# Kernel optimization log

Hardware: AMD Instinct MI355X
Metric: run time of the kernel (lower is better)

The kernel has to match this reference:

```python
import jax, jax.numpy as jnp
import numpy as np

GAMMA = 1.0
T = 2.0
EPS = 1e-8

def setup_inputs() -> dict:
    key = jax.random.key(0)
    k1, k2 = jax.random.split(key)
    N, D = 8192, 64
    user_vecs = jax.random.normal(k1, (N, D), dtype=jnp.float32)
    item_vecs = jax.random.normal(k2, (N, D), dtype=jnp.float32)
    return {"user_vecs": user_vecs, "item_vecs": item_vecs}

def _normalize(x):
    return x / jnp.linalg.norm(x, axis=-1, keepdims=True)

def _alignment(u, i):
    u = _normalize(u)
    i = _normalize(i)
    return jnp.mean(jnp.sum((u - i) ** 2, axis=1))

def _uniformity(x):
    # log( mean_{i<j} exp(-t * ||x_i - x_j||^2) + eps ) with normalized x.
    # For unit vectors ||x_i - x_j||^2 = 2 - 2 <x_i, x_j>. Use full symmetric
    # Gram matrix: sum over off-diagonal = 2 * sum over i<j; diag contributes
    # exp(0) = 1 per row, so subtract N, divide by N*(N-1).
    x = _normalize(x)
    n = x.shape[0]
    gram = x @ x.T                       # [N, N]
    sq_pdist = jnp.maximum(2.0 - 2.0 * gram, 0.0)
    total = jnp.sum(jnp.exp(-T * sq_pdist))
    mean_pair = (total - n) / (n * (n - 1))
    return jnp.log(mean_pair + EPS)

def reference(user_vecs, item_vecs):
    align = _alignment(user_vecs, item_vecs)
    uniform = GAMMA * (_uniformity(user_vecs) + _uniformity(item_vecs)) / 2.0
    return align + uniform
```

## Files before the change

### kernel.cpp

```cpp
#include <hip/hip_runtime.h>
#include <cstdint>


#define NROWS 8192
#define DIM 64
#define NT2 32
#define GRAM_SLOTS (NT2 * (NT2 + 1))
#define K1_BLOCKS 512

static constexpr float EXP_SCALE = 5.770780163555852f;
static constexpr float EPS_F = 1e-8f;

typedef __bf16 bf16x8 __attribute__((ext_vector_type(8)));
typedef float f32x4 __attribute__((ext_vector_type(4)));

__device__ __forceinline__ unsigned short f32_to_bf16_rn(float f) {
    union { float f; uint32_t u; } c; c.f = f;
    uint32_t u = c.u;
    uint32_t r = u + 0x7FFFu + ((u >> 16) & 1u);
    return (unsigned short)(r >> 16);
}

__global__ void __launch_bounds__(256) normalize_align_kernel(
    const float* __restrict__ user, const float* __restrict__ item,
    unsigned short* __restrict__ xu, unsigned short* __restrict__ xi,
    float* __restrict__ pa)
{
    const int wave = threadIdx.x >> 6;
    const int lane = threadIdx.x & 63;
    const int wid  = blockIdx.x * 4 + wave;

    float asum = 0.0f;
    #pragma unroll
    for (int r = 0; r < 4; ++r) {
        const int idx = (wid * 4 + r) * DIM + lane;
        float u = user[idx];
        float v = item[idx];
        float su = u * u, sv = v * v;
        #pragma unroll
        for (int m = 1; m < 64; m <<= 1) {
            su += __shfl_xor(su, m, 64);
            sv += __shfl_xor(sv, m, 64);
        }
        float iu = rsqrtf(su); iu = iu * (1.5f - 0.5f * su * iu * iu);
        float iv = rsqrtf(sv); iv = iv * (1.5f - 0.5f * sv * iv * iv);
        float un = u * iu, vn = v * iv;
        xu[idx] = f32_to_bf16_rn(un);
        xi[idx] = f32_to_bf16_rn(vn);
        float d = un - vn;
        asum += d * d;
    }
    #pragma unroll
    for (int m = 1; m < 64; m <<= 1) asum += __shfl_xor(asum, m, 64);
    __shared__ float ws4[4];
    if (lane == 0) ws4[wave] = asum;
    __syncthreads();
    if (threadIdx.x == 0) pa[blockIdx.x] = ws4[0] + ws4[1] + ws4[2] + ws4[3];
}

__global__ void __launch_bounds__(512, 8) gram_exp_kernel(
    const unsigned short* __restrict__ xu,
    const unsigned short* __restrict__ xi,
    float* __restrict__ pg)
{
    const int bx = blockIdx.x, by = blockIdx.y;
    const unsigned short* __restrict__ X;
    int bi, bj;
    if (by < NT2) {
        if (by >= bx) { X = xu; bi = bx; bj = by; }
        else          { X = xi; bi = by; bj = bx; }
    } else            { X = xi; bi = bx; bj = bx; }
    const bool diag = (bi == bj);

    __shared__ unsigned short lds[16384];
    __shared__ float wsum[8];

    const int wave = threadIdx.x >> 6;
    const int lane = threadIdx.x & 63;

    bf16x8 a[2][2];
    {
        const int arow = bi * 256 + wave * 32 + (lane & 15);
        const int acol = (lane >> 4) * 8;
        #pragma unroll
        for (int rb = 0; rb < 2; ++rb)
            #pragma unroll
            for (int ks = 0; ks < 2; ++ks)
                a[rb][ks] = *reinterpret_cast<const bf16x8*>(
                    X + (arow + rb * 16) * DIM + acol + ks * 32);
    }

    {
        const int base = bj * 256;
        #pragma unroll
        for (int i = 0; i < 4; ++i) {
            int n = i * 512 + threadIdx.x;
            int r = n >> 3, c = n & 7;
            bf16x8 v = *reinterpret_cast<const bf16x8*>(X + (base + r) * DIM + c * 8);
            int di = (r >> 4) * 1024 + c * 128 + (r & 15) * 8;
            *reinterpret_cast<bf16x8*>(&lds[di]) = v;
        }
    }
    __syncthreads();

    float l0 = 0.0f, l1 = 0.0f;
    #pragma unroll
    for (int cb = 0; cb < 16; ++cb) {
        bf16x8 b0 = *reinterpret_cast<const bf16x8*>(&lds[cb * 1024 + lane * 8]);
        bf16x8 b1 = *reinterpret_cast<const bf16x8*>(&lds[cb * 1024 + 512 + lane * 8]);
        #pragma unroll
        for (int rb = 0; rb < 2; ++rb) {
            f32x4 c = {0.f, 0.f, 0.f, 0.f};
            c = __builtin_amdgcn_mfma_f32_16x16x32_bf16(a[rb][0], b0, c, 0, 0, 0);
            c = __builtin_amdgcn_mfma_f32_16x16x32_bf16(a[rb][1], b1, c, 0, 0, 0);
            #pragma unroll
            for (int e = 0; e < 4; ++e) {
                float ex = __builtin_amdgcn_exp2f(fmaf(c[e], EXP_SCALE, -EXP_SCALE));
                if (diag) ex = fminf(ex, 1.0f);
                if (e & 1) l1 += ex; else l0 += ex;
            }
        }
    }

    float local = l0 + l1;
    #pragma unroll
    for (int m = 1; m < 64; m <<= 1) local += __shfl_xor(local, m, 64);
    if (lane == 0) wsum[wave] = local;
    __syncthreads();
    if (threadIdx.x == 0) {
        float t = 0.f;
        #pragma unroll
        for (int w = 0; w < 8; ++w) t += wsum[w];
        pg[by * NT2 + bx] = diag ? t : 2.0f * t;
    }
}

__global__ void __launch_bounds__(256) final_kernel(
    const float* __restrict__ pa, const float* __restrict__ pg,
    float* __restrict__ out)
{
    float a = 0.f, su = 0.f, si = 0.f;
    for (int s = threadIdx.x; s < K1_BLOCKS; s += 256) a += pa[s];
    for (int s = threadIdx.x; s < GRAM_SLOTS; s += 256) {
        int bx = s & (NT2 - 1), by = s >> 5;
        bool is_item = (by == NT2) || (by < bx);
        float v = pg[s];
        if (is_item) si += v; else su += v;
    }
    #pragma unroll
    for (int m = 1; m < 64; m <<= 1) {
        a  += __shfl_xor(a,  m, 64);
        su += __shfl_xor(su, m, 64);
        si += __shfl_xor(si, m, 64);
    }
    __shared__ float r[12];
    const int wave = threadIdx.x >> 6, lane = threadIdx.x & 63;
    if (lane == 0) { r[wave] = a; r[4 + wave] = su; r[8 + wave] = si; }
    __syncthreads();
    if (threadIdx.x == 0) {
        float A  = r[0] + r[1] + r[2]  + r[3];
        float SU = r[4] + r[5] + r[6]  + r[7];
        float SI = r[8] + r[9] + r[10] + r[11];
        const float n = (float)NROWS;
        const float denom = n * (n - 1.0f);
        out[0] = A / n + 0.5f * (logf((SU - n) / denom + EPS_F)
                               + logf((SI - n) / denom + EPS_F));
    }
}

extern "C" void kernel_launch(void* const* d_in, const int* in_sizes, int n_in,
                              void* d_out, int out_size, void* d_ws, size_t ws_size,
                              hipStream_t stream)
{
    const float* user = (const float*)d_in[0];
    const float* item = (const float*)d_in[1];

    unsigned short* xu = (unsigned short*)d_ws;
    unsigned short* xi = xu + (size_t)NROWS * DIM;
    float* pa = (float*)(xi + (size_t)NROWS * DIM);
    float* pg = pa + K1_BLOCKS;

    normalize_align_kernel<<<K1_BLOCKS, 256, 0, stream>>>(user, item, xu, xi, pa);
    gram_exp_kernel<<<dim3(NT2, NT2 + 1), 512, 0, stream>>>(xu, xi, pg);
    final_kernel<<<1, 256, 0, stream>>>(pa, pg, (float*)d_out);
}
```

Baseline: 83.80 us.

## Fuse normalization and alignment into gram kernel, dropping separate normalize pass

Removes the standalone normalize/align kernel and its bf16 workspace round-trip. Each gram block now loads fp32 rows directly, computes norms with lane shuffles and converts to bf16 in registers before the MFMA step. The diagonal item blocks (moved to row 0 of the grid) also compute the alignment term against user rows. This saves one launch and intermediate traffic, but every row is normalized redundantly by about 32 blocks and fp32 loads are twice the bytes of bf16.

```diff
diff --git a/kernel.cpp b/kernel.cpp
--- a/kernel.cpp
+++ b/kernel.cpp
@@ -5,8 +5,7 @@
 #define NROWS 8192
 #define DIM 64
 #define NT2 32
-#define GRAM_SLOTS (NT2 * (NT2 + 1))
-#define K1_BLOCKS 512
+#define NBLK (NT2 * (NT2 + 1))
 
 static constexpr float EXP_SCALE = 5.770780163555852f;
 static constexpr float EPS_F = 1e-8f;
@@ -14,91 +13,106 @@
 typedef __bf16 bf16x8 __attribute__((ext_vector_type(8)));
 typedef float f32x4 __attribute__((ext_vector_type(4)));
 
-__device__ __forceinline__ unsigned short f32_to_bf16_rn(float f) {
-    union { float f; uint32_t u; } c; c.f = f;
-    uint32_t u = c.u;
-    uint32_t r = u + 0x7FFFu + ((u >> 16) & 1u);
-    return (unsigned short)(r >> 16);
-}
-
-__global__ void __launch_bounds__(256) normalize_align_kernel(
+__device__ __forceinline__ float rsq_nr(float s) {
+    float r = rsqrtf(s);
+    return r * (1.5f - 0.5f * s * r * r);
+}
+__device__ __forceinline__ float dot4(float4 a) {
+    return a.x * a.x + a.y * a.y + a.z * a.z + a.w * a.w;
+}
+
+__global__ void __launch_bounds__(512, 8) gram_fused_kernel(
     const float* __restrict__ user, const float* __restrict__ item,
-    unsigned short* __restrict__ xu, unsigned short* __restrict__ xi,
-    float* __restrict__ pa)
-{
-    const int wave = threadIdx.x >> 6;
-    const int lane = threadIdx.x & 63;
-    const int wid  = blockIdx.x * 4 + wave;
-
-    float asum = 0.0f;
-    #pragma unroll
-    for (int r = 0; r < 4; ++r) {
-        const int idx = (wid * 4 + r) * DIM + lane;
-        float u = user[idx];
-        float v = item[idx];
-        float su = u * u, sv = v * v;
-        #pragma unroll
-        for (int m = 1; m < 64; m <<= 1) {
-            su += __shfl_xor(su, m, 64);
-            sv += __shfl_xor(sv, m, 64);
-        }
-        float iu = rsqrtf(su); iu = iu * (1.5f - 0.5f * su * iu * iu);
-        float iv = rsqrtf(sv); iv = iv * (1.5f - 0.5f * sv * iv * iv);
-        float un = u * iu, vn = v * iv;
-        xu[idx] = f32_to_bf16_rn(un);
-        xi[idx] = f32_to_bf16_rn(vn);
-        float d = un - vn;
-        asum += d * d;
-    }
-    #pragma unroll
-    for (int m = 1; m < 64; m <<= 1) asum += __shfl_xor(asum, m, 64);
-    __shared__ float ws4[4];
-    if (lane == 0) ws4[wave] = asum;
-    __syncthreads();
-    if (threadIdx.x == 0) pa[blockIdx.x] = ws4[0] + ws4[1] + ws4[2] + ws4[3];
-}
-
-__global__ void __launch_bounds__(512, 8) gram_exp_kernel(
-    const unsigned short* __restrict__ xu,
-    const unsigned short* __restrict__ xi,
+    float* __restrict__ pa,
     float* __restrict__ pg)
 {
     const int bx = blockIdx.x, by = blockIdx.y;
-    const unsigned short* __restrict__ X;
+    const float* __restrict__ Xf;
     int bi, bj;
-    if (by < NT2) {
-        if (by >= bx) { X = xu; bi = bx; bj = by; }
-        else          { X = xi; bi = by; bj = bx; }
-    } else            { X = xi; bi = bx; bj = bx; }
+    bool align_blk = false;
+    if (by == 0) { Xf = item; bi = bx; bj = bx; align_blk = true; }
+    else {
+        const int yy = by - 1;
+        if (yy >= bx) { Xf = user; bi = bx; bj = yy; }
+        else          { Xf = item; bi = yy; bj = bx; }
+    }
     const bool diag = (bi == bj);
 
     __shared__ unsigned short lds[16384];
-    __shared__ float wsum[8];
+    float* wsum = reinterpret_cast<float*>(lds);
 
     const int wave = threadIdx.x >> 6;
     const int lane = threadIdx.x & 63;
 
     bf16x8 a[2][2];
     {
-        const int arow = bi * 256 + wave * 32 + (lane & 15);
-        const int acol = (lane >> 4) * 8;
-        #pragma unroll
-        for (int rb = 0; rb < 2; ++rb)
-            #pragma unroll
-            for (int ks = 0; ks < 2; ++ks)
-                a[rb][ks] = *reinterpret_cast<const bf16x8*>(
-                    X + (arow + rb * 16) * DIM + acol + ks * 32);
-    }
-
+        const int r16 = lane & 15, q = lane >> 4;
+        const int arow = bi * 256 + wave * 32 + r16;
+        #pragma unroll
+        for (int rb = 0; rb < 2; ++rb) {
+            const float* gp = Xf + (arow + rb * 16) * DIM + q * 8;
+            float4 x0 = *reinterpret_cast<const float4*>(gp);
+            float4 x1 = *reinterpret_cast<const float4*>(gp + 4);
+            float4 y0 = *reinterpret_cast<const float4*>(gp + 32);
+            float4 y1 = *reinterpret_cast<const float4*>(gp + 36);
+            float ss = dot4(x0) + dot4(x1) + dot4(y0) + dot4(y1);
+            ss += __shfl_xor(ss, 16, 64);
+            ss += __shfl_xor(ss, 32, 64);
+            const float rs = rsq_nr(ss);
+            bf16x8 f0, f1;
+            f0[0] = (__bf16)(x0.x * rs); f0[1] = (__bf16)(x0.y * rs);
+            f0[2] = (__bf16)(x0.z * rs); f0[3] = (__bf16)(x0.w * rs);
+            f0[4] = (__bf16)(x1.x * rs); f0[5] = (__bf16)(x1.y * rs);
+            f0[6] = (__bf16)(x1.z * rs); f0[7] = (__bf16)(x1.w * rs);
+            f1[0] = (__bf16)(y0.x * rs); f1[1] = (__bf16)(y0.y * rs);
+            f1[2] = (__bf16)(y0.z * rs); f1[3] = (__bf16)(y0.w * rs);
+            f1[4] = (__bf16)(y1.x * rs); f1[5] = (__bf16)(y1.y * rs);
+            f1[6] = (__bf16)(y1.z * rs); f1[7] = (__bf16)(y1.w * rs);
+            a[rb][0] = f0; a[rb][1] = f1;
+        }
+    }
+
+    float asum = 0.0f;
     {
         const int base = bj * 256;
         #pragma unroll
         for (int i = 0; i < 4; ++i) {
-            int n = i * 512 + threadIdx.x;
-            int r = n >> 3, c = n & 7;
-            bf16x8 v = *reinterpret_cast<const bf16x8*>(X + (base + r) * DIM + c * 8);
-            int di = (r >> 4) * 1024 + c * 128 + (r & 15) * 8;
-            *reinterpret_cast<bf16x8*>(&lds[di]) = v;
+            const int n = i * 512 + threadIdx.x;
+            const int r = n >> 3, c = n & 7;
+            const float* gp = Xf + (base + r) * DIM + c * 8;
+            float4 v0 = *reinterpret_cast<const float4*>(gp);
+            float4 v1 = *reinterpret_cast<const float4*>(gp + 4);
+            float ss = dot4(v0) + dot4(v1);
+            ss += __shfl_xor(ss, 1, 64);
+            ss += __shfl_xor(ss, 2, 64);
+            ss += __shfl_xor(ss, 4, 64);
+            const float rs = rsq_nr(ss);
+            bf16x8 f;
+            f[0] = (__bf16)(v0.x * rs); f[1] = (__bf16)(v0.y * rs);
+            f[2] = (__bf16)(v0.z * rs); f[3] = (__bf16)(v0.w * rs);
+            f[4] = (__bf16)(v1.x * rs); f[5] = (__bf16)(v1.y * rs);
+            f[6] = (__bf16)(v1.z * rs); f[7] = (__bf16)(v1.w * rs);
+            const int di = (r >> 4) * 1024 + c * 128 + (r & 15) * 8;
+            *reinterpret_cast<bf16x8*>(&lds[di]) = f;
+            if (align_blk) {
+                const float* up = user + (base + r) * DIM + c * 8;
+                float4 u0 = *reinterpret_cast<const float4*>(up);
+                float4 u1 = *reinterpret_cast<const float4*>(up + 4);
+                float us = dot4(u0) + dot4(u1);
+                us += __shfl_xor(us, 1, 64);
+                us += __shfl_xor(us, 2, 64);
+                us += __shfl_xor(us, 4, 64);
+                const float urs = rsq_nr(us);
+                float d;
+                d = u0.x * urs - v0.x * rs; asum += d * d;
+                d = u0.y * urs - v0.y * rs; asum += d * d;
+                d = u0.z * urs - v0.z * rs; asum += d * d;
+                d = u0.w * urs - v0.w * rs; asum += d * d;
+                d = u1.x * urs - v1.x * rs; asum += d * d;
+                d = u1.y * urs - v1.y * rs; asum += d * d;
+                d = u1.z * urs - v1.z * rs; asum += d * d;
+                d = u1.w * urs - v1.w * rs; asum += d * d;
+            }
         }
     }
     __syncthreads();
@@ -125,13 +139,19 @@
     float local = l0 + l1;
     #pragma unroll
     for (int m = 1; m < 64; m <<= 1) local += __shfl_xor(local, m, 64);
-    if (lane == 0) wsum[wave] = local;
+    if (align_blk) {
+        #pragma unroll
+        for (int m = 1; m < 64; m <<= 1) asum += __shfl_xor(asum, m, 64);
+    }
+    __syncthreads();
+    if (lane == 0) { wsum[wave] = local; wsum[8 + wave] = asum; }
     __syncthreads();
     if (threadIdx.x == 0) {
-        float t = 0.f;
-        #pragma unroll
-        for (int w = 0; w < 8; ++w) t += wsum[w];
+        float t = 0.f, A = 0.f;
+        #pragma unroll
+        for (int w = 0; w < 8; ++w) { t += wsum[w]; A += wsum[8 + w]; }
         pg[by * NT2 + bx] = diag ? t : 2.0f * t;
+        if (align_blk) pa[bx] = A;
     }
 }
 
@@ -140,12 +160,11 @@
     float* __restrict__ out)
 {
     float a = 0.f, su = 0.f, si = 0.f;
-    for (int s = threadIdx.x; s < K1_BLOCKS; s += 256) a += pa[s];
-    for (int s = threadIdx.x; s < GRAM_SLOTS; s += 256) {
-        int bx = s & (NT2 - 1), by = s >> 5;
-        bool is_item = (by == NT2) || (by < bx);
-        float v = pg[s];
-        if (is_item) si += v; else su += v;
+    if (threadIdx.x < NT2) a = pa[threadIdx.x];
+    for (int s = threadIdx.x; s < NBLK; s += 256) {
+        const int px = s & (NT2 - 1), py = s >> 5;
+        const float v = pg[s];
+        if (py != 0 && (py - 1) >= px) su += v; else si += v;
     }
     #pragma unroll
     for (int m = 1; m < 64; m <<= 1) {
@@ -175,12 +194,9 @@
     const float* user = (const float*)d_in[0];
     const float* item = (const float*)d_in[1];
 
-    unsigned short* xu = (unsigned short*)d_ws;
-    unsigned short* xi = xu + (size_t)NROWS * DIM;
-    float* pa = (float*)(xi + (size_t)NROWS * DIM);
-    float* pg = pa + K1_BLOCKS;
-
-    normalize_align_kernel<<<K1_BLOCKS, 256, 0, stream>>>(user, item, xu, xi, pa);
-    gram_exp_kernel<<<dim3(NT2, NT2 + 1), 512, 0, stream>>>(xu, xi, pg);
+    float* pa = (float*)d_ws;
+    float* pg = pa + NT2;
+
+    gram_fused_kernel<<<dim3(NT2, NT2 + 1), 512, 0, stream>>>(user, item, pa, pg);
     final_kernel<<<1, 256, 0, stream>>>(pa, pg, (float*)d_out);
 }
```

Measured after the change: 90.32 us. 1.08x slower.

## Fuse final reduction into gram kernel via last-block atomics; vectorize normalize

Applied to the files above, without the earlier changes.

Drops the separate final reduction kernel. Each gram block now atomically adds its partial sum into one of 32 slots, and the last block to finish, found with an atomic counter, computes the final scalar. The normalize kernel now has each 16-lane group handle a whole row with float4 loads and ushort4 stores, which removes the per-row 64-lane shuffle reductions. It also zeroes the atomic slots for the next kernel. This saves a kernel launch and its serialization gap, at the cost of atomic contention and float summation order that varies between runs.

```diff
diff --git a/kernel.cpp b/kernel.cpp
--- a/kernel.cpp
+++ b/kernel.cpp
@@ -5,8 +5,9 @@
 #define NROWS 8192
 #define DIM 64
 #define NT2 32
-#define GRAM_SLOTS (NT2 * (NT2 + 1))
+#define NBLK (NT2 * (NT2 + 1))
 #define K1_BLOCKS 512
+#define PA_SLOTS (K1_BLOCKS * 4)
 
 static constexpr float EXP_SCALE = 5.770780163555852f;
 static constexpr float EPS_F = 1e-8f;
@@ -20,48 +21,66 @@
     uint32_t r = u + 0x7FFFu + ((u >> 16) & 1u);
     return (unsigned short)(r >> 16);
 }
+__device__ __forceinline__ float rsq_nr(float s) {
+    float r = rsqrtf(s);
+    return r * (1.5f - 0.5f * s * r * r);
+}
+__device__ __forceinline__ float dot4(float4 a) {
+    return a.x * a.x + a.y * a.y + a.z * a.z + a.w * a.w;
+}
 
 __global__ void __launch_bounds__(256) normalize_align_kernel(
     const float* __restrict__ user, const float* __restrict__ item,
     unsigned short* __restrict__ xu, unsigned short* __restrict__ xi,
-    float* __restrict__ pa)
+    float* __restrict__ pa, float* __restrict__ gsum)
 {
     const int wave = threadIdx.x >> 6;
     const int lane = threadIdx.x & 63;
-    const int wid  = blockIdx.x * 4 + wave;
+    const int row  = blockIdx.x * 16 + wave * 4 + (lane >> 4);
+    const int col4 = (lane & 15) * 4;
+    const int off  = row * DIM + col4;
+
+    float4 u4 = *reinterpret_cast<const float4*>(user + off);
+    float4 v4 = *reinterpret_cast<const float4*>(item + off);
+
+    float su = dot4(u4), sv = dot4(v4);
+    #pragma unroll
+    for (int m = 1; m < 16; m <<= 1) {
+        su += __shfl_xor(su, m, 64);
+        sv += __shfl_xor(sv, m, 64);
+    }
+    const float iu = rsq_nr(su), iv = rsq_nr(sv);
+
+    float un[4] = { u4.x * iu, u4.y * iu, u4.z * iu, u4.w * iu };
+    float vn[4] = { v4.x * iv, v4.y * iv, v4.z * iv, v4.w * iv };
+
+    ushort4 ou, oi;
+    ou.x = f32_to_bf16_rn(un[0]); ou.y = f32_to_bf16_rn(un[1]);
+    ou.z = f32_to_bf16_rn(un[2]); ou.w = f32_to_bf16_rn(un[3]);
+    oi.x = f32_to_bf16_rn(vn[0]); oi.y = f32_to_bf16_rn(vn[1]);
+    oi.z = f32_to_bf16_rn(vn[2]); oi.w = f32_to_bf16_rn(vn[3]);
+    *reinterpret_cast<ushort4*>(xu + off) = ou;
+    *reinterpret_cast<ushort4*>(xi + off) = oi;
 
     float asum = 0.0f;
     #pragma unroll
-    for (int r = 0; r < 4; ++r) {
-        const int idx = (wid * 4 + r) * DIM + lane;
-        float u = user[idx];
-        float v = item[idx];
-        float su = u * u, sv = v * v;
-        #pragma unroll
-        for (int m = 1; m < 64; m <<= 1) {
-            su += __shfl_xor(su, m, 64);
-            sv += __shfl_xor(sv, m, 64);
-        }
-        float iu = rsqrtf(su); iu = iu * (1.5f - 0.5f * su * iu * iu);
-        float iv = rsqrtf(sv); iv = iv * (1.5f - 0.5f * sv * iv * iv);
-        float un = u * iu, vn = v * iv;
-        xu[idx] = f32_to_bf16_rn(un);
-        xi[idx] = f32_to_bf16_rn(vn);
-        float d = un - vn;
-        asum += d * d;
-    }
+    for (int e = 0; e < 4; ++e) { float d = un[e] - vn[e]; asum += d * d; }
     #pragma unroll
     for (int m = 1; m < 64; m <<= 1) asum += __shfl_xor(asum, m, 64);
-    __shared__ float ws4[4];
-    if (lane == 0) ws4[wave] = asum;
-    __syncthreads();
-    if (threadIdx.x == 0) pa[blockIdx.x] = ws4[0] + ws4[1] + ws4[2] + ws4[3];
+    if (lane == 0) pa[blockIdx.x * 4 + wave] = asum;
+
+    if (blockIdx.x == 0) {
+        if (threadIdx.x < 32) gsum[threadIdx.x] = 0.0f;
+        if (threadIdx.x == 32) reinterpret_cast<int*>(gsum + 32)[0] = 0;
+    }
 }
 
 __global__ void __launch_bounds__(512, 8) gram_exp_kernel(
     const unsigned short* __restrict__ xu,
     const unsigned short* __restrict__ xi,
-    float* __restrict__ pg)
+    const float* __restrict__ pa,
+    float* __restrict__ gsum,
+    float* __restrict__ out)
 {
     const int bx = blockIdx.x, by = blockIdx.y;
     const unsigned short* __restrict__ X;
@@ -71,9 +90,11 @@
         else          { X = xi; bi = by; bj = bx; }
     } else            { X = xi; bi = bx; bj = bx; }
     const bool diag = (bi == bj);
+    const int  cat  = (by < NT2 && by >= bx) ? 0 : 1;
 
     __shared__ unsigned short lds[16384];
-    __shared__ float wsum[8];
+    float* fsh = reinterpret_cast<float*>(lds);
+    __shared__ int lastflag;
 
     const int wave = threadIdx.x >> 6;
     const int lane = threadIdx.x & 63;
@@ -125,46 +146,50 @@
     float local = l0 + l1;
     #pragma unroll
     for (int m = 1; m < 64; m <<= 1) local += __shfl_xor(local, m, 64);
-    if (lane == 0) wsum[wave] = local;
+    __syncthreads();
+    if (lane == 0) fsh[wave] = local;
     __syncthreads();
     if (threadIdx.x == 0) {
         float t = 0.f;
         #pragma unroll
-        for (int w = 0; w < 8; ++w) t += wsum[w];
-        pg[by * NT2 + bx] = diag ? t : 2.0f * t;
-    }
-}
-
-__global__ void __launch_bounds__(256) final_kernel(
-    const float* __restrict__ pa, const float* __restrict__ pg,
-    float* __restrict__ out)
-{
-    float a = 0.f, su = 0.f, si = 0.f;
-    for (int s = threadIdx.x; s < K1_BLOCKS; s += 256) a += pa[s];
-    for (int s = threadIdx.x; s < GRAM_SLOTS; s += 256) {
-        int bx = s & (NT2 - 1), by = s >> 5;
-        bool is_item = (by == NT2) || (by < bx);
-        float v = pg[s];
-        if (is_item) si += v; else su += v;
-    }
-    #pragma unroll
-    for (int m = 1; m < 64; m <<= 1) {
-        a  += __shfl_xor(a,  m, 64);
-        su += __shfl_xor(su, m, 64);
-        si += __shfl_xor(si, m, 64);
-    }
-    __shared__ float r[12];
-    const int wave = threadIdx.x >> 6, lane = threadIdx.x & 63;
-    if (lane == 0) { r[wave] = a; r[4 + wave] = su; r[8 + wave] = si; }
-    __syncthreads();
-    if (threadIdx.x == 0) {
-        float A  = r[0] + r[1] + r[2]  + r[3];
-        float SU = r[4] + r[5] + r[6]  + r[7];
-        float SI = r[8] + r[9] + r[10] + r[11];
-        const float n = (float)NROWS;
-        const float denom = n * (n - 1.0f);
-        out[0] = A / n + 0.5f * (logf((SU - n) / denom + EPS_F)
-                               + logf((SI - n) / denom + EPS_F));
+        for (int w = 0; w < 8; ++w) t += fsh[w];
+        if (!diag) t *= 2.0f;
+        atomicAdd(&gsum[cat * 16 + (bx & 15)], t);
+        __threadfence();
+        int old = atomicAdd(reinterpret_cast<int*>(gsum + 32), 1);
+        lastflag = (old == NBLK - 1);
+    }
+    __syncthreads();
+
+    if (lastflag) {
+        __threadfence();
+        float a_ = 0.f;
+        for (int s = threadIdx.x; s < PA_SLOTS; s += 512) a_ += pa[s];
+        float su_ = 0.f, si_ = 0.f;
+        if (threadIdx.x < 16)                         su_ = atomicAdd(&gsum[threadIdx.x], 0.0f);
+        else if (threadIdx.x < 32)                    si_ = atomicAdd(&gsum[threadIdx.x], 0.0f);
+        #pragma unroll
+        for (int m = 1; m < 64; m <<= 1) {
+            a_  += __shfl_xor(a_,  m, 64);
+            su_ += __shfl_xor(su_, m, 64);
+            si_ += __shfl_xor(si_, m, 64);
+        }
+        __syncthreads();
+        if (lane == 0) {
+            fsh[wave] = a_; fsh[8 + wave] = su_; fsh[16 + wave] = si_;
+        }
+        __syncthreads();
+        if (threadIdx.x == 0) {
+            float A = 0.f, SU = 0.f, SI = 0.f;
+            #pragma unroll
+            for (int w = 0; w < 8; ++w) {
+                A += fsh[w]; SU += fsh[8 + w]; SI += fsh[16 + w];
+            }
+            const float n = (float)NROWS;
+            const float denom = n * (n - 1.0f);
+            out[0] = A / n + 0.5f * (logf((SU - n) / denom + EPS_F)
+                                   + logf((SI - n) / denom + EPS_F));
+        }
     }
 }
 
@@ -177,10 +202,9 @@
 
     unsigned short* xu = (unsigned short*)d_ws;
     unsigned short* xi = xu + (size_t)NROWS * DIM;
-    float* pa = (float*)(xi + (size_t)NROWS * DIM);
-    float* pg = pa + K1_BLOCKS;
-
-    normalize_align_kernel<<<K1_BLOCKS, 256, 0, stream>>>(user, item, xu, xi, pa);
-    gram_exp_kernel<<<dim3(NT2, NT2 + 1), 512, 0, stream>>>(xu, xi, pg);
-    final_kernel<<<1, 256, 0, stream>>>(pa, pg, (float*)d_out);
-}
+    float* pa   = (float*)(xi + (size_t)NROWS * DIM);
+    float* gsum = pa + PA_SLOTS;
+
+    normalize_align_kernel<<<K1_BLOCKS, 256, 0, stream>>>(user, item, xu, xi, pa, gsum);
+    gram_exp_kernel<<<dim3(NT2, NT2 + 1), 512, 0, stream>>>(xu, xi, pa, gsum, (float*)d_out);
+}
```

Result: slower. 88.54 us (+5.7%).

## Store normalized bf16 vectors in MFMA fragment layout and vectorize normalization

Applied to the files above, without the earlier changes.

The normalize kernel now loads float4 per lane, reduces row norms across 16 lanes, and writes the bf16 outputs directly in the 16-row MFMA fragment layout. The gram kernel can then load A fragments and the B tile with contiguous 16-byte copies, with no per-element index remapping. The normalize kernel also drops its LDS reduction and writes per-wave partials, and the gram kernel reuses its LDS tile buffer for the final sum. This changes how the workspace is laid out and touches all three kernels, in exchange for cheaper memory access and less address arithmetic.

```diff
diff --git a/kernel.cpp b/kernel.cpp
--- a/kernel.cpp
+++ b/kernel.cpp
@@ -7,6 +7,7 @@
 #define NT2 32
 #define GRAM_SLOTS (NT2 * (NT2 + 1))
 #define K1_BLOCKS 512
+#define PA_SLOTS (K1_BLOCKS * 4)
 
 static constexpr float EXP_SCALE = 5.770780163555852f;
 static constexpr float EPS_F = 1e-8f;
@@ -20,6 +21,13 @@
     uint32_t r = u + 0x7FFFu + ((u >> 16) & 1u);
     return (unsigned short)(r >> 16);
 }
+__device__ __forceinline__ float rsq_nr(float s) {
+    float r = rsqrtf(s);
+    return r * (1.5f - 0.5f * s * r * r);
+}
+__device__ __forceinline__ float dot4(float4 a) {
+    return a.x * a.x + a.y * a.y + a.z * a.z + a.w * a.w;
+}
 
 __global__ void __launch_bounds__(256) normalize_align_kernel(
     const float* __restrict__ user, const float* __restrict__ item,
@@ -28,34 +36,39 @@
 {
     const int wave = threadIdx.x >> 6;
     const int lane = threadIdx.x & 63;
-    const int wid  = blockIdx.x * 4 + wave;
+    const int row  = blockIdx.x * 16 + wave * 4 + (lane >> 4);
+    const int col4 = (lane & 15) * 4;
+    const int off  = row * DIM + col4;
+
+    float4 u4 = *reinterpret_cast<const float4*>(user + off);
+    float4 v4 = *reinterpret_cast<const float4*>(item + off);
+
+    float su = dot4(u4), sv = dot4(v4);
+    #pragma unroll
+    for (int m = 1; m < 16; m <<= 1) {
+        su += __shfl_xor(su, m, 64);
+        sv += __shfl_xor(sv, m, 64);
+    }
+    const float iu = rsq_nr(su), iv = rsq_nr(sv);
+
+    float un[4] = { u4.x * iu, u4.y * iu, u4.z * iu, u4.w * iu };
+    float vn[4] = { v4.x * iv, v4.y * iv, v4.z * iv, v4.w * iv };
+
+    const int fidx = (row >> 4) * 1024 + (col4 >> 3) * 128 + (row & 15) * 8 + (col4 & 7);
+    ushort4 ou, oi;
+    ou.x = f32_to_bf16_rn(un[0]); ou.y = f32_to_bf16_rn(un[1]);
+    ou.z = f32_to_bf16_rn(un[2]); ou.w = f32_to_bf16_rn(un[3]);
+    oi.x = f32_to_bf16_rn(vn[0]); oi.y = f32_to_bf16_rn(vn[1]);
+    oi.z = f32_to_bf16_rn(vn[2]); oi.w = f32_to_bf16_rn(vn[3]);
+    *reinterpret_cast<ushort4*>(xu + fidx) = ou;
+    *reinterpret_cast<ushort4*>(xi + fidx) = oi;
 
     float asum = 0.0f;
     #pragma unroll
-    for (int r = 0; r < 4; ++r) {
-        const int idx = (wid * 4 + r) * DIM + lane;
-        float u = user[idx];
-        float v = item[idx];
-        float su = u * u, sv = v * v;
-        #pragma unroll
-        for (int m = 1; m < 64; m <<= 1) {
-            su += __shfl_xor(su, m, 64);
-            sv += __shfl_xor(sv, m, 64);
-        }
-        float iu = rsqrtf(su); iu = iu * (1.5f - 0.5f * su * iu * iu);
-        float iv = rsqrtf(sv); iv = iv * (1.5f - 0.5f * sv * iv * iv);
-        float un = u * iu, vn = v * iv;
-        xu[idx] = f32_to_bf16_rn(un);
-        xi[idx] = f32_to_bf16_rn(vn);
-        float d = un - vn;
-        asum += d * d;
-    }
+    for (int e = 0; e < 4; ++e) { float d = un[e] - vn[e]; asum += d * d; }
     #pragma unroll
     for (int m = 1; m < 64; m <<= 1) asum += __shfl_xor(asum, m, 64);
-    __shared__ float ws4[4];
-    if (lane == 0) ws4[wave] = asum;
-    __syncthreads();
-    if (threadIdx.x == 0) pa[blockIdx.x] = ws4[0] + ws4[1] + ws4[2] + ws4[3];
+    if (lane == 0) pa[blockIdx.x * 4 + wave] = asum;
 }
 
 __global__ void __launch_bounds__(512, 8) gram_exp_kernel(
@@ -73,32 +86,28 @@
     const bool diag = (bi == bj);
 
     __shared__ unsigned short lds[16384];
-    __shared__ float wsum[8];
+    float* fsh = reinterpret_cast<float*>(lds);
 
     const int wave = threadIdx.x >> 6;
     const int lane = threadIdx.x & 63;
 
     bf16x8 a[2][2];
     {
-        const int arow = bi * 256 + wave * 32 + (lane & 15);
-        const int acol = (lane >> 4) * 8;
+        const unsigned short* ab = X + (bi * 16 + wave * 2) * 1024 + lane * 8;
         #pragma unroll
         for (int rb = 0; rb < 2; ++rb)
             #pragma unroll
             for (int ks = 0; ks < 2; ++ks)
-                a[rb][ks] = *reinterpret_cast<const bf16x8*>(
-                    X + (arow + rb * 16) * DIM + acol + ks * 32);
+                a[rb][ks] = *reinterpret_cast<const bf16x8*>(ab + rb * 1024 + ks * 512);
     }
 
     {
-        const int base = bj * 256;
+        const unsigned short* sb = X + bj * 16384;
         #pragma unroll
         for (int i = 0; i < 4; ++i) {
-            int n = i * 512 + threadIdx.x;
-            int r = n >> 3, c = n & 7;
-            bf16x8 v = *reinterpret_cast<const bf16x8*>(X + (base + r) * DIM + c * 8);
-            int di = (r >> 4) * 1024 + c * 128 + (r & 15) * 8;
-            *reinterpret_cast<bf16x8*>(&lds[di]) = v;
+            const int n = i * 512 + threadIdx.x;
+            *reinterpret_cast<bf16x8*>(&lds[n * 8]) =
+                *reinterpret_cast<const bf16x8*>(sb + n * 8);
         }
     }
     __syncthreads();
@@ -125,12 +134,13 @@
     float local = l0 + l1;
     #pragma unroll
     for (int m = 1; m < 64; m <<= 1) local += __shfl_xor(local, m, 64);
-    if (lane == 0) wsum[wave] = local;
+    __syncthreads();
+    if (lane == 0) fsh[wave] = local;
     __syncthreads();
     if (threadIdx.x == 0) {
         float t = 0.f;
         #pragma unroll
-        for (int w = 0; w < 8; ++w) t += wsum[w];
+        for (int w = 0; w < 8; ++w) t += fsh[w];
         pg[by * NT2 + bx] = diag ? t : 2.0f * t;
     }
 }
@@ -140,11 +150,11 @@
     float* __restrict__ out)
 {
     float a = 0.f, su = 0.f, si = 0.f;
-    for (int s = threadIdx.x; s < K1_BLOCKS; s += 256) a += pa[s];
+    for (int s = threadIdx.x; s < PA_SLOTS; s += 256) a += pa[s];
     for (int s = threadIdx.x; s < GRAM_SLOTS; s += 256) {
-        int bx = s & (NT2 - 1), by = s >> 5;
-        bool is_item = (by == NT2) || (by < bx);
-        float v = pg[s];
+        const int px = s & (NT2 - 1), py = s >> 5;
+        const bool is_item = (py == NT2) || (py < px);
+        const float v = pg[s];
         if (is_item) si += v; else su += v;
     }
     #pragma unroll
@@ -178,7 +188,7 @@
     unsigned short* xu = (unsigned short*)d_ws;
     unsigned short* xi = xu + (size_t)NROWS * DIM;
     float* pa = (float*)(xi + (size_t)NROWS * DIM);
-    float* pg = pa + K1_BLOCKS;
+    float* pg = pa + PA_SLOTS;
 
     normalize_align_kernel<<<K1_BLOCKS, 256, 0, stream>>>(user, item, xu, xi, pa);
     gram_exp_kernel<<<dim3(NT2, NT2 + 1), 512, 0, stream>>>(xu, xi, pg);
```

After: 85.95 us. 1.03x slower.
